# Kernel tuning notes

Hardware: AMD Instinct MI355X
Metric: run time of the kernel (lower is better)

## Reference

```python
import jax, jax.numpy as jnp
import numpy as np

B, S = 2, 2048
DIM_IN, DIM_OUT, NUM_HEADS, DIM_QK = 1024, 128, 16, 128


def setup_inputs() -> dict:
    key = jax.random.key(0)
    k0, k1, k2, k3 = jax.random.split(key, 4)
    x = jax.random.normal(k0, (B, S, DIM_IN), jnp.float32)
    mask = jax.random.bernoulli(k1, 0.1, (B, S))  # True = masked-out token
    # xavier-normal-ish scales (exact init values are irrelevant for correctness)
    std_in = float(np.sqrt(2.0 / (NUM_HEADS * DIM_QK + DIM_IN * DIM_QK)))
    proj_in = jax.random.normal(k2, (DIM_IN, NUM_HEADS, 2 * DIM_QK + DIM_OUT), jnp.float32) * std_in
    v_bias = jnp.zeros((NUM_HEADS, DIM_OUT), jnp.float32)
    std_out = float(np.sqrt(2.0 / (DIM_OUT * DIM_OUT + NUM_HEADS * DIM_OUT)))
    proj_out = jax.random.normal(k3, (NUM_HEADS, DIM_OUT, DIM_OUT), jnp.float32) * std_out
    proj_out_bias = jnp.zeros((DIM_OUT,), jnp.float32)
    return {"x": x, "mask": mask, "proj_in": proj_in, "v_bias": v_bias,
            "proj_out": proj_out, "proj_out_bias": proj_out_bias}


def _rotary(t):
    # t: [z, s, h, d]; GPT-NeoX style rotary as in the torch Rotary module
    d = t.shape[-1]
    half = -(-d // 2)  # ceil(d/2), matches torch.arange(0,-1,-2/d)
    freq_half = 10000.0 ** (jnp.arange(half, dtype=jnp.float32) * (-2.0 / d))
    freq = jnp.concatenate([freq_half, freq_half[: half - d % 2]])  # length d
    pos = jnp.arange(t.shape[1], dtype=jnp.float32)
    ang = pos[:, None] * freq[None, :]             # [s, d]
    cos = jnp.cos(ang)[None, :, None, :]
    sin = jnp.sin(ang)[None, :, None, :]
    x1, x2 = jnp.split(t, 2, axis=-1)
    rot = jnp.concatenate([-x2, x1], axis=-1)
    return t * cos + rot * sin


def _inf_cube(t):
    return t ** 3


def reference(x, mask, proj_in, v_bias, proj_out, proj_out_bias):
    qkv = jnp.einsum('zki,iho->zkho', x, proj_in)
    q, k, v = jnp.split(qkv, [DIM_QK, 2 * DIM_QK], axis=-1)
    q = _rotary(q)
    k = _rotary(k)
    scores = jnp.einsum('zqha,zkha->zqkh', q, k) / jnp.sqrt(jnp.float32(DIM_QK))
    # dual mask: row (query) OR column (key) masked -> -inf
    m = jnp.logical_or(mask[:, :, None, None], mask[:, None, :, None])  # [z,q,k,1]
    scores = jnp.where(m, -jnp.inf, scores)
    attn = jnp.nan_to_num(jax.nn.softmax(scores, axis=2))  # softmax over k; nan rows -> 0
    o = jnp.einsum('zqkh,zkhx->zqhx', attn, v + v_bias[None, None])
    out = jnp.einsum('zqhx,hxy->zqy', _inf_cube(o), proj_out) + proj_out_bias[None, None]
    return _inf_cube(out)
```

## Files before the change

### kernel.cpp

```cpp
#include <hip/hip_runtime.h>
#include <math.h>

#define BZ 2
#define SQ 2048
#define DIN 1024
#define HH 16
#define NT 6144
#define MROWS 4096
#define KOUT 2048
#define KSPLIT 8

typedef unsigned short u16t;
typedef unsigned int u32t;
typedef __attribute__((ext_vector_type(8))) short bf16x8;
typedef __attribute__((ext_vector_type(4))) float f32x4;

__device__ __forceinline__ float cubef(float x) { return x * x * x; }

__device__ __forceinline__ u16t f2bf(float f) {
    u32t b = __float_as_uint(f);
    b += 0x7FFFu + ((b >> 16) & 1u);
    return (u16t)(b >> 16);
}
__device__ __forceinline__ float bf2f(u16t u) { return __uint_as_float(((u32t)u) << 16); }
__device__ __forceinline__ u32t pk2(float a, float b) {
    return (u32t)f2bf(a) | ((u32t)f2bf(b) << 16);
}

__global__ __launch_bounds__(256) void bf16_x(const float* __restrict__ x,
                                              u16t* __restrict__ xb) {
    const size_t idx = ((size_t)blockIdx.x * 256 + threadIdx.x) * 8;
    float4 f0 = *(const float4*)&x[idx];
    float4 f1 = *(const float4*)&x[idx + 4];
    u32t h[4];
    h[0] = pk2(f0.x, f0.y); h[1] = pk2(f0.z, f0.w);
    h[2] = pk2(f1.x, f1.y); h[3] = pk2(f1.z, f1.w);
    *(uint4*)&xb[idx] = *(uint4*)&h[0];
}

__global__ __launch_bounds__(256) void transpose_w(const float* __restrict__ W,
                                                   u16t* __restrict__ Th) {
    __shared__ float tile[64][68];
    const int n0 = blockIdx.x * 64;
    const int k0 = blockIdx.y * 64;
    const int t = threadIdx.x;
    {
        const int r = t >> 4, c = (t & 15) * 4;
        #pragma unroll
        for (int p = 0; p < 4; p++) {
            float4 v = *(const float4*)&W[(size_t)(k0 + r + p * 16) * NT + n0 + c];
            *(float4*)&tile[r + p * 16][c] = v;
        }
    }
    __syncthreads();
    const int nr = t >> 2;
    const int kc = (t & 3) * 16;
    u32t hi[8];
    #pragma unroll
    for (int j = 0; j < 8; j++)
        hi[j] = pk2(tile[kc + 2 * j][nr], tile[kc + 2 * j + 1][nr]);
    size_t ob = (size_t)(n0 + nr) * DIN + k0 + kc;
    *(uint4*)&Th[ob]     = *(uint4*)&hi[0];
    *(uint4*)&Th[ob + 8] = *(uint4*)&hi[4];
}

__global__ __launch_bounds__(256) void transpose_w2(const float* __restrict__ W,
                                                    u16t* __restrict__ Th) {
    __shared__ float tile[64][68];
    const int n0 = blockIdx.x * 64;
    const int k0 = blockIdx.y * 64;
    const int t = threadIdx.x;
    {
        const int r = t >> 4, c = (t & 15) * 4;
        #pragma unroll
        for (int p = 0; p < 4; p++) {
            float4 v = *(const float4*)&W[(size_t)(k0 + r + p * 16) * 128 + n0 + c];
            *(float4*)&tile[r + p * 16][c] = v;
        }
    }
    __syncthreads();
    const int nr = t >> 2;
    const int kc = (t & 3) * 16;
    u32t hi[8];
    #pragma unroll
    for (int j = 0; j < 8; j++)
        hi[j] = pk2(tile[kc + 2 * j][nr], tile[kc + 2 * j + 1][nr]);
    size_t ob = (size_t)(n0 + nr) * KOUT + k0 + kc;
    *(uint4*)&Th[ob]     = *(uint4*)&hi[0];
    *(uint4*)&Th[ob + 8] = *(uint4*)&hi[4];
}

__global__ __launch_bounds__(256) void gemm_qkv3(const u16t* __restrict__ Ah,
                                                 const u16t* __restrict__ Bh,
                                                 const float* __restrict__ vb,
                                                 u16t* __restrict__ QB,
                                                 u16t* __restrict__ KB,
                                                 u16t* __restrict__ VF) {
    __shared__ __align__(16) u16t as_h[4 * 128 * 8];
    __shared__ __align__(16) u16t bs_h[4 * 128 * 8];

    const int t = threadIdx.x;
    const int lane = t & 63, wid = t >> 6;
    const int quad = lane >> 4, l15 = lane & 15;
    const int wm = (wid & 1) * 64;
    const int wn = (wid >> 1) * 64;
    const int tile = blockIdx.x;
    const int h = tile / 3, t3 = tile - h * 3;
    const int colBase = tile * 128;
    const int rowBase = blockIdx.y * 128;
    const int sm = t & 127;
    const int skh = t >> 7;

    f32x4 acc[4][4];
    #pragma unroll
    for (int i = 0; i < 4; i++)
        #pragma unroll
        for (int j = 0; j < 4; j++) acc[i][j] = (f32x4){0.f, 0.f, 0.f, 0.f};

    const u16t* aPtr = Ah + (size_t)(rowBase + sm) * DIN + skh * 16;
    const u16t* bPtr = Bh + (size_t)(colBase + sm) * DIN + skh * 16;
    u16t* aw = &as_h[(skh * 2) * 1024 + sm * 8];
    u16t* bw = &bs_h[(skh * 2) * 1024 + sm * 8];

    for (int k0 = 0; k0 < DIN; k0 += 32) {
        uint4 a0 = *(const uint4*)(aPtr + k0);
        uint4 a1 = *(const uint4*)(aPtr + k0 + 8);
        uint4 b0 = *(const uint4*)(bPtr + k0);
        uint4 b1 = *(const uint4*)(bPtr + k0 + 8);
        __syncthreads();
        *(uint4*)(aw)        = a0;
        *(uint4*)(aw + 1024) = a1;
        *(uint4*)(bw)        = b0;
        *(uint4*)(bw + 1024) = b1;
        __syncthreads();

        bf16x8 ah[4], bh[4];
        #pragma unroll
        for (int mt = 0; mt < 4; mt++)
            ah[mt] = *(const bf16x8*)&as_h[quad * 1024 + (wm + mt * 16 + l15) * 8];
        #pragma unroll
        for (int nt = 0; nt < 4; nt++)
            bh[nt] = *(const bf16x8*)&bs_h[quad * 1024 + (wn + nt * 16 + l15) * 8];
        #pragma unroll
        for (int mt = 0; mt < 4; mt++)
            #pragma unroll
            for (int nt = 0; nt < 4; nt++)
                acc[mt][nt] = __builtin_amdgcn_mfma_f32_16x16x32_bf16(ah[mt], bh[nt], acc[mt][nt], 0, 0, 0);
    }

    const int z = rowBase >> 11;
    const int s0 = (rowBase & 2047) + wm + quad * 4;
    const size_t obase = (size_t)(z * 16 + h) * 2048;
    if (t3 == 2) {
        #pragma unroll
        for (int nt = 0; nt < 4; nt++) {
            int c = wn + nt * 16 + l15;
            float bb = vb[h * 128 + c];
            #pragma unroll
            for (int mt = 0; mt < 4; mt++)
                #pragma unroll
                for (int r = 0; r < 4; r++)
                    VF[(obase + s0 + mt * 16 + r) * 128 + c] = f2bf(acc[mt][nt][r] + bb);
        }
    } else {
        u16t* dst = t3 ? KB : QB;
        #pragma unroll
        for (int nt = 0; nt < 4; nt++) {
            int c = wn + nt * 16 + l15;
            #pragma unroll
            for (int mt = 0; mt < 4; mt++)
                #pragma unroll
                for (int r = 0; r < 4; r++)
                    dst[(obase + s0 + mt * 16 + r) * 128 + c] = f2bf(acc[mt][nt][r]);
        }
    }
}

__global__ __launch_bounds__(256) void prep_rot_trans(u16t* __restrict__ QB,
                                                      u16t* __restrict__ KB,
                                                      u16t* __restrict__ VTh) {
    const int bx = blockIdx.x;
    const int st = bx & 63, h = (bx >> 6) & 15, z = bx >> 10;
    const int t = threadIdx.x;
    const size_t base = ((size_t)(z * 16 + h) * 2048 + st * 32) * 128;

    {
        const int r = t >> 3, w = t & 7;
        const int c = w & 3;
        const int s = st * 32 + r;
        u16t* buf = (w < 4) ? QB : KB;
        u16t* p1 = buf + base + (size_t)r * 128 + c * 16;
        u16t* p2 = p1 + 64;
        uint4 a0 = *(uint4*)p1, a1 = *(uint4*)(p1 + 8);
        uint4 b0 = *(uint4*)p2, b1 = *(uint4*)(p2 + 8);
        u32t A[8] = {a0.x, a0.y, a0.z, a0.w, a1.x, a1.y, a1.z, a1.w};
        u32t B[8] = {b0.x, b0.y, b0.z, b0.w, b1.x, b1.y, b1.z, b1.w};
        u32t OA[8], OB[8];
        #pragma unroll
        for (int p = 0; p < 8; p++) {
            float x1a = bf2f((u16t)(A[p] & 0xFFFFu)), x1b = bf2f((u16t)(A[p] >> 16));
            float x2a = bf2f((u16t)(B[p] & 0xFFFFu)), x2b = bf2f((u16t)(B[p] >> 16));
            int j0 = c * 16 + 2 * p;
            float f0 = expf(-0.14391156831212788f * (float)j0);
            float f1 = expf(-0.14391156831212788f * (float)(j0 + 1));
            float sn0, cs0, sn1, cs1;
            sincosf((float)s * f0, &sn0, &cs0);
            sincosf((float)s * f1, &sn1, &cs1);
            OA[p] = pk2(x1a * cs0 - x2a * sn0, x1b * cs1 - x2b * sn1);
            OB[p] = pk2(x2a * cs0 + x1a * sn0, x2b * cs1 + x1b * sn1);
        }
        *(uint4*)p1       = make_uint4(OA[0], OA[1], OA[2], OA[3]);
        *(uint4*)(p1 + 8) = make_uint4(OA[4], OA[5], OA[6], OA[7]);
        *(uint4*)p2       = make_uint4(OB[0], OB[1], OB[2], OB[3]);
        *(uint4*)(p2 + 8) = make_uint4(OB[4], OB[5], OB[6], OB[7]);
    }

    __shared__ u16t vt[128 * 40];
    {
        uint4 a = *(uint4*)(VTh + base + t * 16);
        uint4 b = *(uint4*)(VTh + base + t * 16 + 8);
        int row = t >> 3, d0 = (t & 7) * 16;
        u32t W[8] = {a.x, a.y, a.z, a.w, b.x, b.y, b.z, b.w};
        #pragma unroll
        for (int p = 0; p < 8; p++) {
            vt[(d0 + 2 * p) * 40 + row]     = (u16t)(W[p] & 0xFFFFu);
            vt[(d0 + 2 * p + 1) * 40 + row] = (u16t)(W[p] >> 16);
        }
    }
    __syncthreads();
    {
        int d = t >> 1, k0 = (t & 1) * 16;
        uint4 a = *(uint4*)&vt[d * 40 + k0];
        uint4 b = *(uint4*)&vt[d * 40 + k0 + 8];
        *(uint4*)(VTh + base + t * 16)     = a;
        *(uint4*)(VTh + base + t * 16 + 8) = b;
    }
}

#define ATTSCALE 0.08838834764831845f

__global__ __launch_bounds__(256, 2) void attn_kernel5(const u16t* __restrict__ QB,
                                                       const u16t* __restrict__ KB,
                                                       const u16t* __restrict__ VTh,
                                                       const int* __restrict__ mask,
                                                       u16t* __restrict__ O3b) {
    const int blk = blockIdx.x;
    const int qt = blk & 15;
    const int h  = (blk >> 4) & 15;
    const int z  = blk >> 8;
    const int t  = threadIdx.x;
    const int lane = t & 63, wid = t >> 6;
    const int quad = lane >> 4, l15 = lane & 15;

    __shared__ __align__(16) u16t ks[2][32 * 136];
    __shared__ __align__(16) u16t vth[2][128 * 40];
    __shared__ __align__(16) u16t wlb[128 * 40];
    __shared__ int qm[128], km[2][32];

    const int q0 = qt * 128;
    const size_t zh = (size_t)(z * 16 + h);
    const u16t* qb  = QB  + zh * 262144;
    const u16t* kb  = KB  + zh * 262144;
    const u16t* vhg = VTh + zh * 262144;

    bf16x8 qf[2][4];
    #pragma unroll
    for (int i = 0; i < 2; i++)
        #pragma unroll
        for (int kk = 0; kk < 4; kk++)
            qf[i][kk] = *(const bf16x8*)(qb + (size_t)(q0 + 16 * (2 * wid + i) + l15) * 128 + kk * 32 + quad * 8);
    if (t < 128) qm[t] = mask[z * SQ + q0 + t];

    const int srow = t >> 3, sco = (t & 7) * 16;
    const int sdd = t >> 1, sk0 = (t & 1) * 16;

    uint4 ka, kb2, va, vb2;
    int kmv = 0;
    {
        const u16t* src = kb + t * 16;
        ka  = *(const uint4*)(src);
        kb2 = *(const uint4*)(src + 8);
        const u16t* srch = vhg + t * 16;
        va  = *(const uint4*)(srch);
        vb2 = *(const uint4*)(srch + 8);
        if (t < 32) kmv = mask[z * SQ + t];
    }

    f32x4 acc[2][8];
    #pragma unroll
    for (int i = 0; i < 2; i++)
        #pragma unroll
        for (int d = 0; d < 8; d++) acc[i][d] = (f32x4){0.f, 0.f, 0.f, 0.f};
    float dsum[2][4] = {{0.f, 0.f, 0.f, 0.f}, {0.f, 0.f, 0.f, 0.f}};

    for (int it = 0; it < 64; it++) {
        const int buf = it & 1;
        *(uint4*)&ks[buf][srow * 136 + sco]     = ka;
        *(uint4*)&ks[buf][srow * 136 + sco + 8] = kb2;
        *(uint4*)&vth[buf][sdd * 40 + sk0]      = va;
        *(uint4*)&vth[buf][sdd * 40 + sk0 + 8]  = vb2;
        if (t < 32) km[buf][t] = kmv;

        {
            const int ktn = (it < 63) ? (it + 1) * 32 : it * 32;
            const u16t* src = kb + (size_t)ktn * 128 + t * 16;
            ka  = *(const uint4*)(src);
            kb2 = *(const uint4*)(src + 8);
            const u16t* srch = vhg + (size_t)(ktn >> 5) * 4096 + t * 16;
            va  = *(const uint4*)(srch);
            vb2 = *(const uint4*)(srch + 8);
            if (t < 32) kmv = mask[z * SQ + ktn + t];
        }

        __syncthreads();

        f32x4 s4[2][2];
        #pragma unroll
        for (int i = 0; i < 2; i++)
            #pragma unroll
            for (int n = 0; n < 2; n++) s4[i][n] = (f32x4){0.f, 0.f, 0.f, 0.f};
        #pragma unroll
        for (int kk = 0; kk < 4; kk++) {
            bf16x8 kf0 = *(const bf16x8*)&ks[buf][l15 * 136 + kk * 32 + quad * 8];
            bf16x8 kf1 = *(const bf16x8*)&ks[buf][(16 + l15) * 136 + kk * 32 + quad * 8];
            s4[0][0] = __builtin_amdgcn_mfma_f32_16x16x32_bf16(qf[0][kk], kf0, s4[0][0], 0, 0, 0);
            s4[0][1] = __builtin_amdgcn_mfma_f32_16x16x32_bf16(qf[0][kk], kf1, s4[0][1], 0, 0, 0);
            s4[1][0] = __builtin_amdgcn_mfma_f32_16x16x32_bf16(qf[1][kk], kf0, s4[1][0], 0, 0, 0);
            s4[1][1] = __builtin_amdgcn_mfma_f32_16x16x32_bf16(qf[1][kk], kf1, s4[1][1], 0, 0, 0);
        }
        {
            int colm0 = km[buf][l15], colm1 = km[buf][16 + l15];
            #pragma unroll
            for (int i = 0; i < 2; i++)
                #pragma unroll
                for (int r = 0; r < 4; r++) {
                    int row = 16 * (2 * wid + i) + 4 * quad + r;
                    int qmr = qm[row];
                    float w0 = (qmr | colm0) ? 0.f : __expf(s4[i][0][r] * ATTSCALE);
                    float w1 = (qmr | colm1) ? 0.f : __expf(s4[i][1][r] * ATTSCALE);
                    dsum[i][r] += w0 + w1;
                    wlb[row * 40 + l15]      = f2bf(w0);
                    wlb[row * 40 + 16 + l15] = f2bf(w1);
                }
        }
        bf16x8 pa[2];
        #pragma unroll
        for (int i = 0; i < 2; i++)
            pa[i] = *(const bf16x8*)&wlb[(16 * (2 * wid + i) + l15) * 40 + quad * 8];
        #pragma unroll
        for (int dt = 0; dt < 8; dt++) {
            bf16x8 vh = *(const bf16x8*)&vth[buf][(16 * dt + l15) * 40 + quad * 8];
            acc[0][dt] = __builtin_amdgcn_mfma_f32_16x16x32_bf16(pa[0], vh, acc[0][dt], 0, 0, 0);
            acc[1][dt] = __builtin_amdgcn_mfma_f32_16x16x32_bf16(pa[1], vh, acc[1][dt], 0, 0, 0);
        }
    }

    #pragma unroll
    for (int i = 0; i < 2; i++)
        #pragma unroll
        for (int r = 0; r < 4; r++) {
            float v = dsum[i][r];
            v += __shfl_xor(v, 1);
            v += __shfl_xor(v, 2);
            v += __shfl_xor(v, 4);
            v += __shfl_xor(v, 8);
            dsum[i][r] = v;
        }

    #pragma unroll
    for (int i = 0; i < 2; i++)
        #pragma unroll
        for (int r = 0; r < 4; r++) {
            int row = 16 * (2 * wid + i) + 4 * quad + r;
            float den = dsum[i][r];
            float inv = den > 0.f ? 1.f / den : 0.f;
            u16t* dst = O3b + (size_t)(z * SQ + q0 + row) * KOUT + h * 128;
            #pragma unroll
            for (int dt = 0; dt < 8; dt++)
                dst[16 * dt + l15] = f2bf(cubef(acc[i][dt][r] * inv));
        }
}

__global__ __launch_bounds__(256) void final_gemm2(const u16t* __restrict__ Ab,
                                                   const u16t* __restrict__ Bh,
                                                   float* __restrict__ part) {
    __shared__ __align__(16) u16t as_h[4 * 128 * 8];
    __shared__ __align__(16) u16t bs_h[4 * 128 * 8];

    const int t = threadIdx.x;
    const int lane = t & 63, wid = t >> 6;
    const int quad = lane >> 4, l15 = lane & 15;
    const int wm = (wid & 1) * 64;
    const int wn = (wid >> 1) * 64;
    const int rowBase = blockIdx.x * 128;
    const int kBase   = blockIdx.y * (KOUT / KSPLIT);
    const int sm = t & 127;
    const int skh = t >> 7;

    f32x4 acc[4][4];
    #pragma unroll
    for (int i = 0; i < 4; i++)
        #pragma unroll
        for (int j = 0; j < 4; j++) acc[i][j] = (f32x4){0.f, 0.f, 0.f, 0.f};

    const u16t* aPtr = Ab + (size_t)(rowBase + sm) * KOUT + kBase + skh * 16;
    const u16t* bPtr = Bh + (size_t)sm * KOUT + kBase + skh * 16;
    u16t* aw = &as_h[(skh * 2) * 1024 + sm * 8];
    u16t* bw = &bs_h[(skh * 2) * 1024 + sm * 8];

    for (int k0 = 0; k0 < KOUT / KSPLIT; k0 += 32) {
        uint4 a0 = *(const uint4*)(aPtr + k0);
        uint4 a1 = *(const uint4*)(aPtr + k0 + 8);
        uint4 b0 = *(const uint4*)(bPtr + k0);
        uint4 b1 = *(const uint4*)(bPtr + k0 + 8);
        __syncthreads();
        *(uint4*)(aw)        = a0;
        *(uint4*)(aw + 1024) = a1;
        *(uint4*)(bw)        = b0;
        *(uint4*)(bw + 1024) = b1;
        __syncthreads();

        bf16x8 ah[4], bh[4];
        #pragma unroll
        for (int mt = 0; mt < 4; mt++)
            ah[mt] = *(const bf16x8*)&as_h[quad * 1024 + (wm + mt * 16 + l15) * 8];
        #pragma unroll
        for (int nt = 0; nt < 4; nt++)
            bh[nt] = *(const bf16x8*)&bs_h[quad * 1024 + (wn + nt * 16 + l15) * 8];
        #pragma unroll
        for (int mt = 0; mt < 4; mt++)
            #pragma unroll
            for (int nt = 0; nt < 4; nt++)
                acc[mt][nt] = __builtin_amdgcn_mfma_f32_16x16x32_bf16(ah[mt], bh[nt], acc[mt][nt], 0, 0, 0);
    }

    float* pbase = part + (size_t)blockIdx.y * ((size_t)MROWS * 128);
    #pragma unroll
    for (int mt = 0; mt < 4; mt++)
        #pragma unroll
        for (int nt = 0; nt < 4; nt++) {
            int col = wn + nt * 16 + l15;
            #pragma unroll
            for (int r = 0; r < 4; r++) {
                int row = rowBase + wm + mt * 16 + quad * 4 + r;
                pbase[(size_t)row * 128 + col] = acc[mt][nt][r];
            }
        }
}

__global__ __launch_bounds__(256) void reduce_bias_cube(const float* __restrict__ part,
                                                        const float* __restrict__ bias,
                                                        float* __restrict__ out) {
    const int idx = (blockIdx.x * 256 + threadIdx.x) * 4;
    float4 s = {0.f, 0.f, 0.f, 0.f};
    #pragma unroll
    for (int p = 0; p < KSPLIT; p++) {
        float4 v = *(const float4*)&part[(size_t)p * ((size_t)MROWS * 128) + idx];
        s.x += v.x; s.y += v.y; s.z += v.z; s.w += v.w;
    }
    float4 b = *(const float4*)&bias[idx & 127];
    float4 r;
    r.x = cubef(s.x + b.x);
    r.y = cubef(s.y + b.y);
    r.z = cubef(s.z + b.z);
    r.w = cubef(s.w + b.w);
    *(float4*)&out[idx] = r;
}

extern "C" void kernel_launch(void* const* d_in, const int* in_sizes, int n_in,
                              void* d_out, int out_size, void* d_ws, size_t ws_size,
                              hipStream_t stream) {
    const float* x        = (const float*)d_in[0];
    const int*   mask     = (const int*)d_in[1];
    const float* proj_in  = (const float*)d_in[2];
    const float* v_bias   = (const float*)d_in[3];
    const float* proj_out = (const float*)d_in[4];
    const float* po_bias  = (const float*)d_in[5];
    float* out = (float*)d_out;

    u16t* QB  = (u16t*)d_ws;
    u16t* KB  = QB + (size_t)8388608;
    u16t* VTh = KB + (size_t)8388608;
    u16t* xb  = VTh + (size_t)8388608;
    u16t* O3b = xb + (size_t)4194304;
    u16t* pTh = O3b;
    u16t* WTh = QB;
    float* partials = (float*)(WTh + (size_t)128 * KOUT);

    bf16_x<<<(MROWS * DIN) / (256 * 8), 256, 0, stream>>>(x, xb);
    transpose_w<<<dim3(NT / 64, DIN / 64), 256, 0, stream>>>(proj_in, pTh);
    gemm_qkv3<<<dim3(48, MROWS / 128), 256, 0, stream>>>(xb, pTh, v_bias, QB, KB, VTh);
    prep_rot_trans<<<BZ * HH * (SQ / 32), 256, 0, stream>>>(QB, KB, VTh);
    attn_kernel5<<<BZ * HH * (SQ / 128), 256, 0, stream>>>(QB, KB, VTh, mask, O3b);
    transpose_w2<<<dim3(2, KOUT / 64), 256, 0, stream>>>(proj_out, WTh);
    final_gemm2<<<dim3(MROWS / 128, KSPLIT), 256, 0, stream>>>(O3b, WTh, partials);
    reduce_bias_cube<<<(MROWS * 128) / (256 * 4), 256, 0, stream>>>(partials, po_bias, out);
}
```

Measured before the change: 335.1 us.

## Double-buffer GEMM LDS tiles, halve attention query tile, raise split-K

Both bf16 GEMMs (QKV projection and output projection) now keep two LDS buffers. The next K-slice is loaded from global memory while MFMAs run on the current one, which drops one barrier per iteration. The attention kernel moves from 128-row to 64-row query tiles: each wave handles one 16-row slice, the grid doubles and occupancy is hinted at 3 blocks per CU. The output GEMM split-K goes from 8 to 16 for more parallelism. The cost is twice the K/V reloading in attention, twice the partial-sum traffic in the reduction, and more LDS per GEMM block.

```diff
diff --git a/kernel.cpp b/kernel.cpp
--- a/kernel.cpp
+++ b/kernel.cpp
@@ -8,7 +8,7 @@
 #define NT 6144
 #define MROWS 4096
 #define KOUT 2048
-#define KSPLIT 8
+#define KSPLIT 16
 
 typedef unsigned short u16t;
 typedef unsigned int u32t;
@@ -90,14 +90,14 @@
     *(uint4*)&Th[ob + 8] = *(uint4*)&hi[4];
 }
 
-__global__ __launch_bounds__(256) void gemm_qkv3(const u16t* __restrict__ Ah,
+__global__ __launch_bounds__(256) void gemm_qkv4(const u16t* __restrict__ Ah,
                                                  const u16t* __restrict__ Bh,
                                                  const float* __restrict__ vb,
                                                  u16t* __restrict__ QB,
                                                  u16t* __restrict__ KB,
                                                  u16t* __restrict__ VF) {
-    __shared__ __align__(16) u16t as_h[4 * 128 * 8];
-    __shared__ __align__(16) u16t bs_h[4 * 128 * 8];
+    __shared__ __align__(16) u16t as_h[2][4 * 128 * 8];
+    __shared__ __align__(16) u16t bs_h[2][4 * 128 * 8];
 
     const int t = threadIdx.x;
     const int lane = t & 63, wid = t >> 6;
@@ -119,28 +119,34 @@
 
     const u16t* aPtr = Ah + (size_t)(rowBase + sm) * DIN + skh * 16;
     const u16t* bPtr = Bh + (size_t)(colBase + sm) * DIN + skh * 16;
-    u16t* aw = &as_h[(skh * 2) * 1024 + sm * 8];
-    u16t* bw = &bs_h[(skh * 2) * 1024 + sm * 8];
-
-    for (int k0 = 0; k0 < DIN; k0 += 32) {
-        uint4 a0 = *(const uint4*)(aPtr + k0);
-        uint4 a1 = *(const uint4*)(aPtr + k0 + 8);
-        uint4 b0 = *(const uint4*)(bPtr + k0);
-        uint4 b1 = *(const uint4*)(bPtr + k0 + 8);
+    const int swoff = (skh * 2) * 1024 + sm * 8;
+
+    uint4 a0 = *(const uint4*)(aPtr);
+    uint4 a1 = *(const uint4*)(aPtr + 8);
+    uint4 b0 = *(const uint4*)(bPtr);
+    uint4 b1 = *(const uint4*)(bPtr + 8);
+
+    for (int it = 0; it < 32; it++) {
+        const int buf = it & 1;
+        *(uint4*)(&as_h[buf][swoff])        = a0;
+        *(uint4*)(&as_h[buf][swoff + 1024]) = a1;
+        *(uint4*)(&bs_h[buf][swoff])        = b0;
+        *(uint4*)(&bs_h[buf][swoff + 1024]) = b1;
         __syncthreads();
-        *(uint4*)(aw)        = a0;
-        *(uint4*)(aw + 1024) = a1;
-        *(uint4*)(bw)        = b0;
-        *(uint4*)(bw + 1024) = b1;
-        __syncthreads();
-
+        {
+            const int k0 = (it < 31) ? (it + 1) * 32 : it * 32;
+            a0 = *(const uint4*)(aPtr + k0);
+            a1 = *(const uint4*)(aPtr + k0 + 8);
+            b0 = *(const uint4*)(bPtr + k0);
+            b1 = *(const uint4*)(bPtr + k0 + 8);
+        }
         bf16x8 ah[4], bh[4];
         #pragma unroll
         for (int mt = 0; mt < 4; mt++)
-            ah[mt] = *(const bf16x8*)&as_h[quad * 1024 + (wm + mt * 16 + l15) * 8];
+            ah[mt] = *(const bf16x8*)&as_h[buf][quad * 1024 + (wm + mt * 16 + l15) * 8];
         #pragma unroll
         for (int nt = 0; nt < 4; nt++)
-            bh[nt] = *(const bf16x8*)&bs_h[quad * 1024 + (wn + nt * 16 + l15) * 8];
+            bh[nt] = *(const bf16x8*)&bs_h[buf][quad * 1024 + (wn + nt * 16 + l15) * 8];
         #pragma unroll
         for (int mt = 0; mt < 4; mt++)
             #pragma unroll
@@ -239,37 +245,35 @@
 
 #define ATTSCALE 0.08838834764831845f
 
-__global__ __launch_bounds__(256, 2) void attn_kernel5(const u16t* __restrict__ QB,
+__global__ __launch_bounds__(256, 3) void attn_kernel6(const u16t* __restrict__ QB,
                                                        const u16t* __restrict__ KB,
                                                        const u16t* __restrict__ VTh,
                                                        const int* __restrict__ mask,
                                                        u16t* __restrict__ O3b) {
     const int blk = blockIdx.x;
-    const int qt = blk & 15;
-    const int h  = (blk >> 4) & 15;
-    const int z  = blk >> 8;
+    const int qt = blk & 31;
+    const int h  = (blk >> 5) & 15;
+    const int z  = blk >> 9;
     const int t  = threadIdx.x;
     const int lane = t & 63, wid = t >> 6;
     const int quad = lane >> 4, l15 = lane & 15;
 
     __shared__ __align__(16) u16t ks[2][32 * 136];
     __shared__ __align__(16) u16t vth[2][128 * 40];
-    __shared__ __align__(16) u16t wlb[128 * 40];
-    __shared__ int qm[128], km[2][32];
-
-    const int q0 = qt * 128;
+    __shared__ __align__(16) u16t wlb[64 * 40];
+    __shared__ int qm[64], km[2][32];
+
+    const int q0 = qt * 64;
     const size_t zh = (size_t)(z * 16 + h);
     const u16t* qb  = QB  + zh * 262144;
     const u16t* kb  = KB  + zh * 262144;
     const u16t* vhg = VTh + zh * 262144;
 
-    bf16x8 qf[2][4];
-    #pragma unroll
-    for (int i = 0; i < 2; i++)
-        #pragma unroll
-        for (int kk = 0; kk < 4; kk++)
-            qf[i][kk] = *(const bf16x8*)(qb + (size_t)(q0 + 16 * (2 * wid + i) + l15) * 128 + kk * 32 + quad * 8);
-    if (t < 128) qm[t] = mask[z * SQ + q0 + t];
+    bf16x8 qf[4];
+    #pragma unroll
+    for (int kk = 0; kk < 4; kk++)
+        qf[kk] = *(const bf16x8*)(qb + (size_t)(q0 + 16 * wid + l15) * 128 + kk * 32 + quad * 8);
+    if (t < 64) qm[t] = mask[z * SQ + q0 + t];
 
     const int srow = t >> 3, sco = (t & 7) * 16;
     const int sdd = t >> 1, sk0 = (t & 1) * 16;
@@ -277,21 +281,17 @@
     uint4 ka, kb2, va, vb2;
     int kmv = 0;
     {
-        const u16t* src = kb + t * 16;
-        ka  = *(const uint4*)(src);
-        kb2 = *(const uint4*)(src + 8);
-        const u16t* srch = vhg + t * 16;
-        va  = *(const uint4*)(srch);
-        vb2 = *(const uint4*)(srch + 8);
+        ka  = *(const uint4*)(kb + t * 16);
+        kb2 = *(const uint4*)(kb + t * 16 + 8);
+        va  = *(const uint4*)(vhg + t * 16);
+        vb2 = *(const uint4*)(vhg + t * 16 + 8);
         if (t < 32) kmv = mask[z * SQ + t];
     }
 
-    f32x4 acc[2][8];
-    #pragma unroll
-    for (int i = 0; i < 2; i++)
-        #pragma unroll
-        for (int d = 0; d < 8; d++) acc[i][d] = (f32x4){0.f, 0.f, 0.f, 0.f};
-    float dsum[2][4] = {{0.f, 0.f, 0.f, 0.f}, {0.f, 0.f, 0.f, 0.f}};
+    f32x4 acc[8];
+    #pragma unroll
+    for (int d = 0; d < 8; d++) acc[d] = (f32x4){0.f, 0.f, 0.f, 0.f};
+    float dsum[4] = {0.f, 0.f, 0.f, 0.f};
 
     for (int it = 0; it < 64; it++) {
         const int buf = it & 1;
@@ -300,6 +300,8 @@
         *(uint4*)&vth[buf][sdd * 40 + sk0]      = va;
         *(uint4*)&vth[buf][sdd * 40 + sk0 + 8]  = vb2;
         if (t < 32) km[buf][t] = kmv;
+
+        __syncthreads();
 
         {
             const int ktn = (it < 63) ? (it + 1) * 32 : it * 32;
@@ -312,80 +314,61 @@
             if (t < 32) kmv = mask[z * SQ + ktn + t];
         }
 
-        __syncthreads();
-
-        f32x4 s4[2][2];
-        #pragma unroll
-        for (int i = 0; i < 2; i++)
-            #pragma unroll
-            for (int n = 0; n < 2; n++) s4[i][n] = (f32x4){0.f, 0.f, 0.f, 0.f};
+        f32x4 s4[2] = {(f32x4){0.f, 0.f, 0.f, 0.f}, (f32x4){0.f, 0.f, 0.f, 0.f}};
         #pragma unroll
         for (int kk = 0; kk < 4; kk++) {
             bf16x8 kf0 = *(const bf16x8*)&ks[buf][l15 * 136 + kk * 32 + quad * 8];
             bf16x8 kf1 = *(const bf16x8*)&ks[buf][(16 + l15) * 136 + kk * 32 + quad * 8];
-            s4[0][0] = __builtin_amdgcn_mfma_f32_16x16x32_bf16(qf[0][kk], kf0, s4[0][0], 0, 0, 0);
-            s4[0][1] = __builtin_amdgcn_mfma_f32_16x16x32_bf16(qf[0][kk], kf1, s4[0][1], 0, 0, 0);
-            s4[1][0] = __builtin_amdgcn_mfma_f32_16x16x32_bf16(qf[1][kk], kf0, s4[1][0], 0, 0, 0);
-            s4[1][1] = __builtin_amdgcn_mfma_f32_16x16x32_bf16(qf[1][kk], kf1, s4[1][1], 0, 0, 0);
+            s4[0] = __builtin_amdgcn_mfma_f32_16x16x32_bf16(qf[kk], kf0, s4[0], 0, 0, 0);
+            s4[1] = __builtin_amdgcn_mfma_f32_16x16x32_bf16(qf[kk], kf1, s4[1], 0, 0, 0);
         }
         {
             int colm0 = km[buf][l15], colm1 = km[buf][16 + l15];
             #pragma unroll
-            for (int i = 0; i < 2; i++)
-                #pragma unroll
-                for (int r = 0; r < 4; r++) {
-                    int row = 16 * (2 * wid + i) + 4 * quad + r;
-                    int qmr = qm[row];
-                    float w0 = (qmr | colm0) ? 0.f : __expf(s4[i][0][r] * ATTSCALE);
-                    float w1 = (qmr | colm1) ? 0.f : __expf(s4[i][1][r] * ATTSCALE);
-                    dsum[i][r] += w0 + w1;
-                    wlb[row * 40 + l15]      = f2bf(w0);
-                    wlb[row * 40 + 16 + l15] = f2bf(w1);
-                }
-        }
-        bf16x8 pa[2];
-        #pragma unroll
-        for (int i = 0; i < 2; i++)
-            pa[i] = *(const bf16x8*)&wlb[(16 * (2 * wid + i) + l15) * 40 + quad * 8];
+            for (int r = 0; r < 4; r++) {
+                int row = 16 * wid + 4 * quad + r;
+                int qmr = qm[row];
+                float w0 = (qmr | colm0) ? 0.f : __expf(s4[0][r] * ATTSCALE);
+                float w1 = (qmr | colm1) ? 0.f : __expf(s4[1][r] * ATTSCALE);
+                dsum[r] += w0 + w1;
+                wlb[row * 40 + l15]      = f2bf(w0);
+                wlb[row * 40 + 16 + l15] = f2bf(w1);
+            }
+        }
+        bf16x8 pa = *(const bf16x8*)&wlb[(16 * wid + l15) * 40 + quad * 8];
         #pragma unroll
         for (int dt = 0; dt < 8; dt++) {
             bf16x8 vh = *(const bf16x8*)&vth[buf][(16 * dt + l15) * 40 + quad * 8];
-            acc[0][dt] = __builtin_amdgcn_mfma_f32_16x16x32_bf16(pa[0], vh, acc[0][dt], 0, 0, 0);
-            acc[1][dt] = __builtin_amdgcn_mfma_f32_16x16x32_bf16(pa[1], vh, acc[1][dt], 0, 0, 0);
-        }
-    }
-
-    #pragma unroll
-    for (int i = 0; i < 2; i++)
-        #pragma unroll
-        for (int r = 0; r < 4; r++) {
-            float v = dsum[i][r];
-            v += __shfl_xor(v, 1);
-            v += __shfl_xor(v, 2);
-            v += __shfl_xor(v, 4);
-            v += __shfl_xor(v, 8);
-            dsum[i][r] = v;
-        }
-
-    #pragma unroll
-    for (int i = 0; i < 2; i++)
-        #pragma unroll
-        for (int r = 0; r < 4; r++) {
-            int row = 16 * (2 * wid + i) + 4 * quad + r;
-            float den = dsum[i][r];
-            float inv = den > 0.f ? 1.f / den : 0.f;
-            u16t* dst = O3b + (size_t)(z * SQ + q0 + row) * KOUT + h * 128;
-            #pragma unroll
-            for (int dt = 0; dt < 8; dt++)
-                dst[16 * dt + l15] = f2bf(cubef(acc[i][dt][r] * inv));
-        }
-}
-
-__global__ __launch_bounds__(256) void final_gemm2(const u16t* __restrict__ Ab,
+            acc[dt] = __builtin_amdgcn_mfma_f32_16x16x32_bf16(pa, vh, acc[dt], 0, 0, 0);
+        }
+    }
+
+    #pragma unroll
+    for (int r = 0; r < 4; r++) {
+        float v = dsum[r];
+        v += __shfl_xor(v, 1);
+        v += __shfl_xor(v, 2);
+        v += __shfl_xor(v, 4);
+        v += __shfl_xor(v, 8);
+        dsum[r] = v;
+    }
+
+    #pragma unroll
+    for (int r = 0; r < 4; r++) {
+        int row = 16 * wid + 4 * quad + r;
+        float inv = dsum[r] > 0.f ? 1.f / dsum[r] : 0.f;
+        u16t* dst = O3b + (size_t)(z * SQ + q0 + row) * KOUT + h * 128;
+        #pragma unroll
+        for (int dt = 0; dt < 8; dt++)
+            dst[16 * dt + l15] = f2bf(cubef(acc[dt][r] * inv));
+    }
+}
+
+__global__ __launch_bounds__(256) void final_gemm3(const u16t* __restrict__ Ab,
                                                    const u16t* __restrict__ Bh,
                                                    float* __restrict__ part) {
-    __shared__ __align__(16) u16t as_h[4 * 128 * 8];
-    __shared__ __align__(16) u16t bs_h[4 * 128 * 8];
+    __shared__ __align__(16) u16t as_h[2][4 * 128 * 8];
+    __shared__ __align__(16) u16t bs_h[2][4 * 128 * 8];
 
     const int t = threadIdx.x;
     const int lane = t & 63, wid = t >> 6;
@@ -405,28 +388,35 @@
 
     const u16t* aPtr = Ab + (size_t)(rowBase + sm) * KOUT + kBase + skh * 16;
     const u16t* bPtr = Bh + (size_t)sm * KOUT + kBase + skh * 16;
-    u16t* aw = &as_h[(skh * 2) * 1024 + sm * 8];
-    u16t* bw = &bs_h[(skh * 2) * 1024 + sm * 8];
-
-    for (int k0 = 0; k0 < KOUT / KSPLIT; k0 += 32) {
-        uint4 a0 = *(const uint4*)(aPtr + k0);
-        uint4 a1 = *(const uint4*)(aPtr + k0 + 8);
-        uint4 b0 = *(const uint4*)(bPtr + k0);
-        uint4 b1 = *(const uint4*)(bPtr + k0 + 8);
+    const int swoff = (skh * 2) * 1024 + sm * 8;
+
+    uint4 a0 = *(const uint4*)(aPtr);
+    uint4 a1 = *(const uint4*)(aPtr + 8);
+    uint4 b0 = *(const uint4*)(bPtr);
+    uint4 b1 = *(const uint4*)(bPtr + 8);
+
+    const int NIT = (KOUT / KSPLIT) / 32;
+    for (int it = 0; it < NIT; it++) {
+        const int buf = it & 1;
+        *(uint4*)(&as_h[buf][swoff])        = a0;
+        *(uint4*)(&as_h[buf][swoff + 1024]) = a1;
+        *(uint4*)(&bs_h[buf][swoff])        = b0;
+        *(uint4*)(&bs_h[buf][swoff + 1024]) = b1;
         __syncthreads();
-        *(uint4*)(aw)        = a0;
-        *(uint4*)(aw + 1024) = a1;
-        *(uint4*)(bw)        = b0;
-        *(uint4*)(bw + 1024) = b1;
-        __syncthreads();
-
+        {
+            const int k0 = (it < NIT - 1) ? (it + 1) * 32 : it * 32;
+            a0 = *(const uint4*)(aPtr + k0);
+            a1 = *(const uint4*)(aPtr + k0 + 8);
+            b0 = *(const uint4*)(bPtr + k0);
+            b1 = *(const uint4*)(bPtr + k0 + 8);
+        }
         bf16x8 ah[4], bh[4];
         #pragma unroll
         for (int mt = 0; mt < 4; mt++)
-            ah[mt] = *(const bf16x8*)&as_h[quad * 1024 + (wm + mt * 16 + l15) * 8];
+            ah[mt] = *(const bf16x8*)&as_h[buf][quad * 1024 + (wm + mt * 16 + l15) * 8];
         #pragma unroll
         for (int nt = 0; nt < 4; nt++)
-            bh[nt] = *(const bf16x8*)&bs_h[quad * 1024 + (wn + nt * 16 + l15) * 8];
+            bh[nt] = *(const bf16x8*)&bs_h[buf][quad * 1024 + (wn + nt * 16 + l15) * 8];
         #pragma unroll
         for (int mt = 0; mt < 4; mt++)
             #pragma unroll
@@ -489,10 +479,10 @@
 
     bf16_x<<<(MROWS * DIN) / (256 * 8), 256, 0, stream>>>(x, xb);
     transpose_w<<<dim3(NT / 64, DIN / 64), 256, 0, stream>>>(proj_in, pTh);
-    gemm_qkv3<<<dim3(48, MROWS / 128), 256, 0, stream>>>(xb, pTh, v_bias, QB, KB, VTh);
+    gemm_qkv4<<<dim3(48, MROWS / 128), 256, 0, stream>>>(xb, pTh, v_bias, QB, KB, VTh);
     prep_rot_trans<<<BZ * HH * (SQ / 32), 256, 0, stream>>>(QB, KB, VTh);
-    attn_kernel5<<<BZ * HH * (SQ / 128), 256, 0, stream>>>(QB, KB, VTh, mask, O3b);
+    attn_kernel6<<<BZ * HH * (SQ / 64), 256, 0, stream>>>(QB, KB, VTh, mask, O3b);
     transpose_w2<<<dim3(2, KOUT / 64), 256, 0, stream>>>(proj_out, WTh);
-    final_gemm2<<<dim3(MROWS / 128, KSPLIT), 256, 0, stream>>>(O3b, WTh, partials);
+    final_gemm3<<<dim3(MROWS / 128, KSPLIT), 256, 0, stream>>>(O3b, WTh, partials);
     reduce_bias_cube<<<(MROWS * 128) / (256 * 4), 256, 0, stream>>>(partials, po_bias, out);
 }
```

Result: slower. 355.6 us (+6.1%).
